# Optimization experiments

Hardware: AMD Instinct MI355X
Metric: run time of the kernel (lower is better)

The kernel has to match this reference:

```python
import jax, jax.numpy as jnp
import numpy as np

B, S, HID = 2, 2048, 1024
NH, HD = 16, 64
EPS = 1e-12


def setup_inputs() -> dict:
    key = jax.random.key(0)
    ks = jax.random.split(key, 6)
    w_scale = 1.0 / np.sqrt(HID)
    return {
        "hidden_states": jax.random.normal(ks[0], (B, S, HID), dtype=jnp.float32),
        "attention_mask": jnp.ones((B, S), dtype=jnp.float32),
        "Wq": jax.random.normal(ks[1], (HID, HID), dtype=jnp.float32) * w_scale,
        "bq": jnp.zeros((HID,), dtype=jnp.float32),
        "Wk": jax.random.normal(ks[2], (HID, HID), dtype=jnp.float32) * w_scale,
        "bk": jnp.zeros((HID,), dtype=jnp.float32),
        "Wv": jax.random.normal(ks[3], (HID, HID), dtype=jnp.float32) * w_scale,
        "bv": jnp.zeros((HID,), dtype=jnp.float32),
        "Wd": jax.random.normal(ks[4], (HID, HID), dtype=jnp.float32) * w_scale,
        "bd": jnp.zeros((HID,), dtype=jnp.float32),
        "ln_gamma": jnp.ones((HID,), dtype=jnp.float32),
        "ln_beta": jnp.zeros((HID,), dtype=jnp.float32),
    }


def _heads(x):  # [B,S,HID] -> [B,NH,S,HD]
    return x.reshape(B, S, NH, HD).transpose(0, 2, 1, 3)


def reference(hidden_states, attention_mask, Wq, bq, Wk, bk, Wv, bv, Wd, bd, ln_gamma, ln_beta):
    # pre-LayerNorm
    mu = jnp.mean(hidden_states, axis=-1, keepdims=True)
    var = jnp.mean(jnp.square(hidden_states - mu), axis=-1, keepdims=True)
    h = (hidden_states - mu) * jax.lax.rsqrt(var + EPS) * ln_gamma + ln_beta

    q = _heads(h @ Wq.T + bq)  # [B,NH,S,HD]
    k = _heads(h @ Wk.T + bk)
    v = _heads(h @ Wv.T + bv)

    # additive mask: -1000 * (1 - mask), broadcast over heads and query pos
    add_mask = -1000.0 * (1.0 - attention_mask)[:, None, None, :]  # [B,1,1,S]

    # scale applied symmetrically to q and k: sqrt(sqrt(HD)) each
    scale = np.sqrt(np.sqrt(HD)).astype(np.float32)
    scores = jnp.einsum("bhqd,bhkd->bhqk", q / scale, k / scale) + add_mask
    probs = jax.nn.softmax(scores, axis=-1)  # dropout p=0 -> identity
    ctx = jnp.einsum("bhqk,bhkd->bhqd", probs, v)  # [B,NH,S,HD]

    ctx = ctx.transpose(0, 2, 1, 3).reshape(B, S, HID)
    return ctx @ Wd.T + bd
```

## Files before the change

kernel.cpp:

```cpp
#include <hip/hip_runtime.h>
#include <hip/hip_bf16.h>
#include <math.h>

#define BATCH 2
#define SEQ   2048
#define HID   1024
#define NH    16
#define HD    64
#define MROWS (BATCH * SEQ)
#define VSTR  4160

typedef unsigned short u16;
typedef short bf16x8 __attribute__((ext_vector_type(8)));
typedef float f32x4  __attribute__((ext_vector_type(4)));

#define LOG2E 1.4426950408889634f
#define C2    (0.125f * LOG2E)
#define M2F   23.083120f

static __device__ __forceinline__ u16 f2bf(float f) {
    union { float f; unsigned int u; } v; v.f = f;
    unsigned int r = (v.u + 0x7FFF + ((v.u >> 16) & 1)) >> 16;
    return (u16)r;
}

static __device__ __forceinline__ unsigned int pk_bf16(float a, float b) {
    union { __hip_bfloat162 h; unsigned int u; } r;
    float2 f; f.x = a; f.y = b;
    r.h = __float22bfloat162_rn(f);
    return r.u;
}

static __device__ __forceinline__ f32x4 mfma16(bf16x8 a, bf16x8 b, f32x4 c) {
    return __builtin_amdgcn_mfma_f32_16x16x32_bf16(a, b, c, 0, 0, 0);
}

static __device__ __forceinline__ void ldsload16(const void* g, void* l) {
    __builtin_amdgcn_global_load_lds(
        (const __attribute__((address_space(1))) void*)(unsigned long long)(uintptr_t)g,
        (__attribute__((address_space(3))) void*)(unsigned int)(uintptr_t)l,
        16, 0, 0);
}

__global__ __launch_bounds__(256) void prep_kernel(const float* __restrict__ x,
                                                   const float* __restrict__ gamma,
                                                   const float* __restrict__ beta,
                                                   u16* __restrict__ h,
                                                   const float* __restrict__ w0,
                                                   const float* __restrict__ w1,
                                                   const float* __restrict__ w2,
                                                   const float* __restrict__ w3,
                                                   u16* o0, u16* o1, u16* o2, u16* o3,
                                                   const float* __restrict__ maskg,
                                                   float* __restrict__ m2g)
{
    __shared__ float red[8];
    const int t = threadIdx.x;
    if (blockIdx.x >= 8192) {
        const int idx = ((blockIdx.x - 8192) * 256 + t) * 4;
        const float4 m = *(const float4*)(maskg + idx);
        float4 o;
        o.x = fmaf(-1000.0f * (1.0f - m.x), LOG2E, -M2F);
        o.y = fmaf(-1000.0f * (1.0f - m.y), LOG2E, -M2F);
        o.z = fmaf(-1000.0f * (1.0f - m.z), LOG2E, -M2F);
        o.w = fmaf(-1000.0f * (1.0f - m.w), LOG2E, -M2F);
        *(float4*)(m2g + idx) = o;
        return;
    }
    if (blockIdx.x < 4096) {
        const int blk = blockIdx.x;
        const int which = blk >> 10;
        const int lb = blk & 1023;
        const float* src = which == 0 ? w0 : which == 1 ? w1 : which == 2 ? w2 : w3;
        u16* dst = which == 0 ? o0 : which == 1 ? o1 : which == 2 ? o2 : o3;
        const int idx = (lb * 256 + t) * 4;
        const float4 f = *(const float4*)(src + idx);
        union { u16 s[4]; uint2 v; } p;
        p.s[0] = f2bf(f.x); p.s[1] = f2bf(f.y); p.s[2] = f2bf(f.z); p.s[3] = f2bf(f.w);
        *(uint2*)(dst + idx) = p.v;
        return;
    }
    const int row = blockIdx.x - 4096;
    const float4 xv = ((const float4*)(x + (size_t)row * HID))[t];
    float s  = xv.x + xv.y + xv.z + xv.w;
    float ss = xv.x * xv.x + xv.y * xv.y + xv.z * xv.z + xv.w * xv.w;
#pragma unroll
    for (int off = 32; off > 0; off >>= 1) {
        s  += __shfl_down(s, off);
        ss += __shfl_down(ss, off);
    }
    const int wid = t >> 6;
    if ((t & 63) == 0) { red[wid] = s; red[4 + wid] = ss; }
    __syncthreads();
    s  = red[0] + red[1] + red[2] + red[3];
    ss = red[4] + red[5] + red[6] + red[7];
    const float mu   = s * (1.0f / HID);
    const float var  = ss * (1.0f / HID) - mu * mu;
    const float rstd = rsqrtf(var + 1e-12f);
    const float4 g  = ((const float4*)gamma)[t];
    const float4 bb = ((const float4*)beta)[t];
    union { u16 s[4]; uint2 v; } p;
    p.s[0] = f2bf((xv.x - mu) * rstd * g.x + bb.x);
    p.s[1] = f2bf((xv.y - mu) * rstd * g.y + bb.y);
    p.s[2] = f2bf((xv.z - mu) * rstd * g.z + bb.z);
    p.s[3] = f2bf((xv.w - mu) * rstd * g.w + bb.w);
    ((uint2*)(h + (size_t)row * HID))[t] = p.v;
}

static __device__ __forceinline__ void gemm_core(const u16* __restrict__ A,
                                                 const u16* __restrict__ B,
                                                 int K, int bm, int bn,
                                                 u16* As, u16* Bs,
                                                 int wave, int lane,
                                                 f32x4 acc[4][4])
{
    const int l15  = lane & 15;
    const int quad = lane >> 4;
    const int wm = (wave >> 1) * 64;
    const int wn = (wave & 1) * 64;

    const int c1 = wave * 64 + lane;
    const int c2 = c1 + 256;
    const u16* A1 = A + (size_t)(bm + (c1 >> 2)) * K + (c1 & 3) * 8;
    const u16* A2 = A + (size_t)(bm + (c2 >> 2)) * K + (c2 & 3) * 8;
    const u16* B1 = B + (size_t)(bn + (c1 >> 2)) * K + (c1 & 3) * 8;
    const u16* B2 = B + (size_t)(bn + (c2 >> 2)) * K + (c2 & 3) * 8;
    const int o1 = wave * 512;
    const int o2 = 2048 + wave * 512;

    ldsload16(A1, As + o1);
    ldsload16(A2, As + o2);
    ldsload16(B1, Bs + o1);
    ldsload16(B2, Bs + o2);

    const int nstep = K >> 5;
    for (int i = 0; i < nstep; i++) {
        __syncthreads();
        const int cb = (i & 1) * 4096;
        if (i + 1 < nstep) {
            const int nb = ((i + 1) & 1) * 4096;
            const int k0 = (i + 1) * 32;
            ldsload16(A1 + k0, As + nb + o1);
            ldsload16(A2 + k0, As + nb + o2);
            ldsload16(B1 + k0, Bs + nb + o1);
            ldsload16(B2 + k0, Bs + nb + o2);
        }
        bf16x8 af[4], bfr[4];
#pragma unroll
        for (int mt = 0; mt < 4; mt++)
            af[mt] = *(const bf16x8*)&As[cb + (wm + mt * 16 + l15) * 32 + quad * 8];
#pragma unroll
        for (int nt = 0; nt < 4; nt++)
            bfr[nt] = *(const bf16x8*)&Bs[cb + (wn + nt * 16 + l15) * 32 + quad * 8];
#pragma unroll
        for (int mt = 0; mt < 4; mt++)
#pragma unroll
            for (int nt = 0; nt < 4; nt++)
                acc[mt][nt] = mfma16(af[mt], bfr[nt], acc[mt][nt]);
    }
}

__global__ __launch_bounds__(256) void qkv_gemm(const u16* __restrict__ h,
                                                const u16* __restrict__ wq,
                                                const u16* __restrict__ wk,
                                                const u16* __restrict__ wv,
                                                const float* __restrict__ bq,
                                                const float* __restrict__ bk,
                                                const float* __restrict__ bv,
                                                u16* __restrict__ qo,
                                                u16* __restrict__ ko,
                                                u16* __restrict__ vo)
{
    __shared__ u16 As[8192];
    __shared__ u16 Bs[8192];
    const int blk  = blockIdx.x;
    const int wave = threadIdx.x >> 6;
    const int lane = threadIdx.x & 63;
    const int l15  = lane & 15;
    const int quad = lane >> 4;
    const int wm = (wave >> 1) * 64;
    const int wn = (wave & 1) * 64;

    f32x4 acc[4][4];
#pragma unroll
    for (int mt = 0; mt < 4; mt++)
#pragma unroll
        for (int nt = 0; nt < 4; nt++) acc[mt][nt] = (f32x4)0.0f;

    if (blk < 512) {
        const u16* W     = (blk < 256) ? wq : wk;
        const float* bia = (blk < 256) ? bq : bk;
        u16* out         = (blk < 256) ? qo : ko;
        const int local = blk & 255;
        const int bm = (local >> 3) * 128;
        const int bn = (local & 7) * 128;
        gemm_core(h, W, HID, bm, bn, As, Bs, wave, lane, acc);

        float bv4[4];
#pragma unroll
        for (int nt = 0; nt < 4; nt++) bv4[nt] = bia[bn + wn + nt * 16 + l15];
#pragma unroll
        for (int mt = 0; mt < 4; mt++)
#pragma unroll
            for (int r = 0; r < 4; r++) {
                const int m  = bm + wm + mt * 16 + quad * 4 + r;
                const int bI = m >> 11;
                const int sI = m & (SEQ - 1);
#pragma unroll
                for (int nt = 0; nt < 4; nt++) {
                    const int n  = bn + wn + nt * 16 + l15;
                    const int hh = n >> 6;
                    const int d  = n & 63;
                    out[(((size_t)(bI * NH + hh) * SEQ + sI) << 6) + d] =
                        f2bf(acc[mt][nt][r] + bv4[nt]);
                }
            }
    } else {
        const int local = blk - 512;
        const int bm = (local & 7) * 128;
        const int bn = (local >> 3) * 128;
        gemm_core(wv, h, HID, bm, bn, As, Bs, wave, lane, acc);

#pragma unroll
        for (int mt = 0; mt < 4; mt++) {
            const f32x4 bm4 = *(const f32x4*)&bv[bm + wm + mt * 16 + quad * 4];
#pragma unroll
            for (int r = 0; r < 4; r++) {
                const int row = bm + wm + mt * 16 + quad * 4 + r;
#pragma unroll
                for (int nt = 0; nt < 4; nt++) {
                    const int col = bn + wn + nt * 16 + l15;
                    vo[(size_t)row * VSTR + col] = f2bf(acc[mt][nt][r] + bm4[r]);
                }
            }
        }
    }
}

__global__ __launch_bounds__(256) void out_gemm(const u16* __restrict__ ctx,
                                                const u16* __restrict__ wd,
                                                const float* __restrict__ bd,
                                                float* __restrict__ out)
{
    __shared__ u16 As[8192];
    __shared__ u16 Bs[8192];
    const int blk  = blockIdx.x;
    const int wave = threadIdx.x >> 6;
    const int lane = threadIdx.x & 63;
    const int l15  = lane & 15;
    const int quad = lane >> 4;
    const int wm = (wave >> 1) * 64;
    const int wn = (wave & 1) * 64;
    const int bm = (blk >> 3) * 128;
    const int bn = (blk & 7) * 128;

    f32x4 acc[4][4];
#pragma unroll
    for (int mt = 0; mt < 4; mt++)
#pragma unroll
        for (int nt = 0; nt < 4; nt++) acc[mt][nt] = (f32x4)0.0f;

    gemm_core(ctx, wd, HID, bm, bn, As, Bs, wave, lane, acc);

    float bv4[4];
#pragma unroll
    for (int nt = 0; nt < 4; nt++) bv4[nt] = bd[bn + wn + nt * 16 + l15];
#pragma unroll
    for (int mt = 0; mt < 4; mt++)
#pragma unroll
        for (int r = 0; r < 4; r++) {
            const int m = bm + wm + mt * 16 + quad * 4 + r;
#pragma unroll
            for (int nt = 0; nt < 4; nt++) {
                const int n = bn + wn + nt * 16 + l15;
                out[(size_t)m * HID + n] = acc[mt][nt][r] + bv4[nt];
            }
        }
}

__global__ __launch_bounds__(512, 4) void attn_mfma(const u16* __restrict__ qb,
                                                    const u16* __restrict__ kb,
                                                    const u16* __restrict__ vtb,
                                                    const float* __restrict__ m2g,
                                                    u16* __restrict__ ctx)
{
    __shared__ __align__(16) char smem[59392];
    u16 (*Pw)[72] = (u16(*)[72])(smem + 32768 + (threadIdx.x >> 6) * 2304);
    float* mlds = (float*)(smem + 51200);

    const int t    = threadIdx.x;
    const int wave = t >> 6;
    const int lane = t & 63;
    const int l15  = lane & 15;
    const int quad = lane >> 4;

    const int bh = blockIdx.x & 31;
    const int qt = blockIdx.x >> 5;
    const int b  = bh >> 4;
    const int hh = bh & 15;
    const int q0 = qt * 128;

    const size_t headoff = (size_t)(b * NH + hh) * SEQ * HD;
    const u16* kbase = kb + headoff;
    const u16* vbase = vtb + (size_t)(hh * HD) * VSTR + b * SEQ;
    const float* m2b = m2g + b * SEQ;

    ((float4*)mlds)[t] = ((const float4*)m2b)[t];

    bf16x8 Qf[2];
    {
        const int qrow = q0 + wave * 16 + l15;
#pragma unroll
        for (int ks = 0; ks < 2; ks++)
            Qf[ks] = *(const bf16x8*)(qb + headoff + (size_t)qrow * HD + ks * 32 + quad * 8);
    }

    f32x4 O[4];
#pragma unroll
    for (int mt = 0; mt < 4; mt++) O[mt] = (f32x4)0.0f;
    f32x4 Lacc = (f32x4)0.0f;
    bf16x8 ones;
#pragma unroll
    for (int j = 0; j < 8; j++) ones[j] = (short)0x3F80;

    const int srow = lane >> 3;
    const int lcol = (lane & 7) ^ srow;
    const int sw0 = ((quad)     ^ (l15 & 7)) * 8;
    const int sw1 = ((quad + 4) ^ (l15 & 7)) * 8;

    const u16* kp = kbase + (size_t)(wave * 8 + srow) * HD + lcol * 8;
    const u16* vp = vbase + (size_t)(wave * 8 + srow) * VSTR + lcol * 8;

    ldsload16(kp, smem + wave * 1024);
    ldsload16(vp, smem + 16384 + wave * 1024);

    for (int i = 0; i < 32; i++) {
        __syncthreads();
        const int c0 = i * 64;
        const u16* Ks  = (const u16*)(smem + (i & 1) * 8192);
        const u16* Vts = (const u16*)(smem + 16384 + (i & 1) * 8192);
        if (i + 1 < 32) {
            const int cn = c0 + 64;
            char* nbK = smem + ((i + 1) & 1) * 8192;
            char* nbV = smem + 16384 + ((i + 1) & 1) * 8192;
            ldsload16(kp + (size_t)cn * HD, nbK + wave * 1024);
            ldsload16(vp + cn,              nbV + wave * 1024);
        }

        f32x4 St[4];
        __builtin_amdgcn_s_setprio(1);
#pragma unroll
        for (int mt = 0; mt < 4; mt++) {
            const int rb = (mt * 16 + l15) * 64;
            const bf16x8 ka0 = *(const bf16x8*)&Ks[rb + sw0];
            const bf16x8 ka1 = *(const bf16x8*)&Ks[rb + sw1];
            f32x4 a = (f32x4)0.0f;
            a = mfma16(ka0, Qf[0], a);
            a = mfma16(ka1, Qf[1], a);
            St[mt] = a;
        }
        __builtin_amdgcn_s_setprio(0);

#pragma unroll
        for (int mt = 0; mt < 4; mt++) {
            const f32x4 mv = *(const f32x4*)(mlds + c0 + mt * 16 + quad * 4);
            float p0 = __builtin_amdgcn_exp2f(fmaf(St[mt][0], C2, mv[0]));
            float p1 = __builtin_amdgcn_exp2f(fmaf(St[mt][1], C2, mv[1]));
            float p2 = __builtin_amdgcn_exp2f(fmaf(St[mt][2], C2, mv[2]));
            float p3 = __builtin_amdgcn_exp2f(fmaf(St[mt][3], C2, mv[3]));
            uint2 w;
            w.x = pk_bf16(p0, p1);
            w.y = pk_bf16(p2, p3);
            *(uint2*)&Pw[l15][mt * 16 + quad * 4] = w;
        }

        const bf16x8 Pb0 = *(const bf16x8*)&Pw[l15][quad * 8];
        const bf16x8 Pb1 = *(const bf16x8*)&Pw[l15][32 + quad * 8];

        __builtin_amdgcn_s_setprio(1);
#pragma unroll
        for (int mt = 0; mt < 4; mt++) {
            const int rb = (mt * 16 + l15) * 64;
            const bf16x8 va0 = *(const bf16x8*)&Vts[rb + sw0];
            const bf16x8 va1 = *(const bf16x8*)&Vts[rb + sw1];
            O[mt] = mfma16(va0, Pb0, O[mt]);
            O[mt] = mfma16(va1, Pb1, O[mt]);
        }
        Lacc = mfma16(ones, Pb0, Lacc);
        Lacc = mfma16(ones, Pb1, Lacc);
        __builtin_amdgcn_s_setprio(0);
    }

    const float linv = 1.0f / Lacc[0];

    __syncthreads();
    float* Ot = (float*)smem + wave * (16 * 68);
#pragma unroll
    for (int mt = 0; mt < 4; mt++) {
        f32x4 v = O[mt] * linv;
        *(f32x4*)(Ot + l15 * 68 + mt * 16 + quad * 4) = v;
    }
    __syncthreads();
    {
        const int ql  = lane >> 2;
        const int seg = lane & 3;
        const float* srcp = Ot + ql * 68 + seg * 16;
        u16* dstp = ctx + (size_t)(b * SEQ + q0 + wave * 16 + ql) * HID
                        + hh * 64 + seg * 16;
#pragma unroll
        for (int j = 0; j < 2; j++) {
            union { u16 s[8]; uint4 v; } p;
#pragma unroll
            for (int i = 0; i < 8; i++) p.s[i] = f2bf(srcp[j * 8 + i]);
            *(uint4*)(dstp + j * 8) = p.v;
        }
    }
}

extern "C" void kernel_launch(void* const* d_in, const int* in_sizes, int n_in,
                              void* d_out, int out_size, void* d_ws, size_t ws_size,
                              hipStream_t stream)
{
    const float* hs    = (const float*)d_in[0];
    const float* mask  = (const float*)d_in[1];
    const float* Wq    = (const float*)d_in[2];
    const float* bq    = (const float*)d_in[3];
    const float* Wk    = (const float*)d_in[4];
    const float* bk    = (const float*)d_in[5];
    const float* Wv    = (const float*)d_in[6];
    const float* bv    = (const float*)d_in[7];
    const float* Wd    = (const float*)d_in[8];
    const float* bd    = (const float*)d_in[9];
    const float* gamma = (const float*)d_in[10];
    const float* beta  = (const float*)d_in[11];
    float* out = (float*)d_out;

    const size_t NE = (size_t)MROWS * HID;
    u16* ws   = (u16*)d_ws;
    u16* h    = ws;
    u16* qbb  = ws + NE;
    u16* kbb  = qbb + NE;
    u16* vtb  = kbb + NE;
    u16* ctxb = vtb + (size_t)HID * VSTR;
    u16* wqb  = ctxb + NE;
    u16* wkb  = wqb + HID * HID;
    u16* wvb  = wkb + HID * HID;
    u16* wdb  = wvb + HID * HID;
    float* m2 = (float*)(wdb + HID * HID);

    prep_kernel<<<8196, 256, 0, stream>>>(hs, gamma, beta, h,
                                          Wq, Wk, Wv, Wd, wqb, wkb, wvb, wdb,
                                          mask, m2);

    qkv_gemm<<<768, 256, 0, stream>>>(h, wqb, wkb, wvb, bq, bk, bv, qbb, kbb, vtb);

    attn_mfma<<<512, 512, 0, stream>>>(qbb, kbb, vtb, m2, ctxb);

    out_gemm<<<256, 256, 0, stream>>>(ctxb, wdb, bd, out);
}
```

Measured before the change: 205.0 us.

## Remap GEMM block indices across XCDs and halve out_gemm tile width

The QKV GEMM now permutes block indices so consecutive blocks stride across the 8 XCDs, and Q and K tiles for the same output tile are interleaved so they share the same h rows in cache. The output GEMM switches from 128x128 to 128x64 tiles with a new gemm_core64 helper, doubling the grid to 512 blocks to fill more CUs, and applies the same XCD-aware remap. Smaller tiles lower per-block arithmetic intensity and increase A-tile reloads from L2.

New measurement: 199.0 us. 1.03x faster.

```diff
diff --git a/kernel.cpp b/kernel.cpp
--- a/kernel.cpp
+++ b/kernel.cpp
@@ -173,7 +173,7 @@
 {
     __shared__ u16 As[8192];
     __shared__ u16 Bs[8192];
-    const int blk  = blockIdx.x;
+    const int blk  = (blockIdx.x & 7) * 96 + (blockIdx.x >> 3);
     const int wave = threadIdx.x >> 6;
     const int lane = threadIdx.x & 63;
     const int l15  = lane & 15;
@@ -188,12 +188,13 @@
         for (int nt = 0; nt < 4; nt++) acc[mt][nt] = (f32x4)0.0f;
 
     if (blk < 512) {
-        const u16* W     = (blk < 256) ? wq : wk;
-        const float* bia = (blk < 256) ? bq : bk;
-        u16* out         = (blk < 256) ? qo : ko;
-        const int local = blk & 255;
-        const int bm = (local >> 3) * 128;
-        const int bn = (local & 7) * 128;
+        const int proj  = blk & 1;
+        const int pair  = blk >> 1;
+        const u16* W     = proj ? wk : wq;
+        const float* bia = proj ? bk : bq;
+        u16* out         = proj ? ko : qo;
+        const int bm = (pair >> 3) * 128;
+        const int bn = (pair & 7) * 128;
         gemm_core(h, W, HID, bm, bn, As, Bs, wave, lane, acc);
 
         float bv4[4];
@@ -237,43 +238,96 @@
     }
 }
 
-__global__ __launch_bounds__(256) void out_gemm(const u16* __restrict__ ctx,
-                                                const u16* __restrict__ wd,
-                                                const float* __restrict__ bd,
-                                                float* __restrict__ out)
+static __device__ __forceinline__ void gemm_core64(const u16* __restrict__ A,
+                                                   const u16* __restrict__ B,
+                                                   int K, int bm, int bn,
+                                                   u16* As, u16* Bs,
+                                                   int wave, int lane,
+                                                   f32x4 acc[4][2])
+{
+    const int l15  = lane & 15;
+    const int quad = lane >> 4;
+    const int wm = (wave >> 1) * 64;
+    const int wn = (wave & 1) * 32;
+
+    const int c1 = wave * 64 + lane;
+    const int c2 = c1 + 256;
+    const u16* A1 = A + (size_t)(bm + (c1 >> 2)) * K + (c1 & 3) * 8;
+    const u16* A2 = A + (size_t)(bm + (c2 >> 2)) * K + (c2 & 3) * 8;
+    const u16* B1 = B + (size_t)(bn + (c1 >> 2)) * K + (c1 & 3) * 8;
+    const int o1 = wave * 512;
+    const int o2 = 2048 + wave * 512;
+    const int ob = wave * 512;
+
+    ldsload16(A1, As + o1);
+    ldsload16(A2, As + o2);
+    ldsload16(B1, Bs + ob);
+
+    const int nstep = K >> 5;
+    for (int i = 0; i < nstep; i++) {
+        __syncthreads();
+        const int ca = (i & 1) * 4096;
+        const int cbb = (i & 1) * 2048;
+        if (i + 1 < nstep) {
+            const int na = ((i + 1) & 1) * 4096;
+            const int nb = ((i + 1) & 1) * 2048;
+            const int k0 = (i + 1) * 32;
+            ldsload16(A1 + k0, As + na + o1);
+            ldsload16(A2 + k0, As + na + o2);
+            ldsload16(B1 + k0, Bs + nb + ob);
+        }
+        bf16x8 af[4], bfr[2];
+#pragma unroll
+        for (int mt = 0; mt < 4; mt++)
+            af[mt] = *(const bf16x8*)&As[ca + (wm + mt * 16 + l15) * 32 + quad * 8];
+#pragma unroll
+        for (int nt = 0; nt < 2; nt++)
+            bfr[nt] = *(const bf16x8*)&Bs[cbb + (wn + nt * 16 + l15) * 32 + quad * 8];
+#pragma unroll
+        for (int mt = 0; mt < 4; mt++)
+#pragma unroll
+            for (int nt = 0; nt < 2; nt++)
+                acc[mt][nt] = mfma16(af[mt], bfr[nt], acc[mt][nt]);
+    }
+}
+
+__global__ __launch_bounds__(256, 6) void out_gemm(const u16* __restrict__ ctx,
+                                                   const u16* __restrict__ wd,
+                                                   const float* __restrict__ bd,
+                                                   float* __restrict__ out)
 {
     __shared__ u16 As[8192];
-    __shared__ u16 Bs[8192];
-    const int blk  = blockIdx.x;
+    __shared__ u16 Bs[4096];
+    const int blk  = (blockIdx.x & 7) * 64 + (blockIdx.x >> 3);
     const int wave = threadIdx.x >> 6;
     const int lane = threadIdx.x & 63;
     const int l15  = lane & 15;
     const int quad = lane >> 4;
     const int wm = (wave >> 1) * 64;
-    const int wn = (wave & 1) * 64;
-    const int bm = (blk >> 3) * 128;
-    const int bn = (blk & 7) * 128;
-
-    f32x4 acc[4][4];
+    const int wn = (wave & 1) * 32;
+    const int bm = (blk >> 4) * 128;
+    const int bn = (blk & 15) * 64;
+
+    f32x4 acc[4][2];
 #pragma unroll
     for (int mt = 0; mt < 4; mt++)
 #pragma unroll
-        for (int nt = 0; nt < 4; nt++) acc[mt][nt] = (f32x4)0.0f;
-
-    gemm_core(ctx, wd, HID, bm, bn, As, Bs, wave, lane, acc);
-
-    float bv4[4];
-#pragma unroll
-    for (int nt = 0; nt < 4; nt++) bv4[nt] = bd[bn + wn + nt * 16 + l15];
+        for (int nt = 0; nt < 2; nt++) acc[mt][nt] = (f32x4)0.0f;
+
+    gemm_core64(ctx, wd, HID, bm, bn, As, Bs, wave, lane, acc);
+
+    float bv2[2];
+#pragma unroll
+    for (int nt = 0; nt < 2; nt++) bv2[nt] = bd[bn + wn + nt * 16 + l15];
 #pragma unroll
     for (int mt = 0; mt < 4; mt++)
 #pragma unroll
         for (int r = 0; r < 4; r++) {
             const int m = bm + wm + mt * 16 + quad * 4 + r;
 #pragma unroll
-            for (int nt = 0; nt < 4; nt++) {
+            for (int nt = 0; nt < 2; nt++) {
                 const int n = bn + wn + nt * 16 + l15;
-                out[(size_t)m * HID + n] = acc[mt][nt][r] + bv4[nt];
+                out[(size_t)m * HID + n] = acc[mt][nt][r] + bv2[nt];
             }
         }
 }
@@ -456,5 +510,5 @@
 
     attn_mfma<<<512, 512, 0, stream>>>(qbb, kbb, vtb, m2, ctxb);
 
-    out_gemm<<<256, 256, 0, stream>>>(ctxb, wdb, bd, out);
-}
+    out_gemm<<<512, 256, 0, stream>>>(ctxb, wdb, bd, out);
+}
```
